# Kernel tuning notes

Hardware: AMD Instinct MI355X
Metric: run time of the kernel (lower is better)

The kernel has to match this reference:

```python
import jax, jax.numpy as jnp
import numpy as np

IN_DIM, HID, B, T = 64, 256, 256, 512


def setup_inputs() -> dict:
    key = jax.random.key(0)
    ks = jax.random.split(key, 12)
    s_in = 1.0 / np.sqrt(HID)
    d = {
        "x": jax.random.normal(ks[0], (B, T, IN_DIM), dtype=jnp.float32),
        # PyTorch LSTM layer 0 params (gate order i,f,g,o)
        "W_ih0": jax.random.uniform(ks[1], (4 * HID, IN_DIM), jnp.float32, -s_in, s_in),
        "W_hh0": jax.random.uniform(ks[2], (4 * HID, HID), jnp.float32, -s_in, s_in),
        "b_ih0": jax.random.uniform(ks[3], (4 * HID,), jnp.float32, -s_in, s_in),
        "b_hh0": jax.random.uniform(ks[4], (4 * HID,), jnp.float32, -s_in, s_in),
        # layer 1
        "W_ih1": jax.random.uniform(ks[5], (4 * HID, HID), jnp.float32, -s_in, s_in),
        "W_hh1": jax.random.uniform(ks[6], (4 * HID, HID), jnp.float32, -s_in, s_in),
        "b_ih1": jax.random.uniform(ks[7], (4 * HID,), jnp.float32, -s_in, s_in),
        "b_hh1": jax.random.uniform(ks[8], (4 * HID,), jnp.float32, -s_in, s_in),
        # linear head
        "W_head": jax.random.uniform(ks[9], (1, HID), jnp.float32, -s_in, s_in),
        "b_head": jax.random.uniform(ks[10], (1,), jnp.float32, -s_in, s_in),
    }
    return d


def _lstm_layer(x, W_ih, W_hh, b_ih, b_hh):
    """x: [B,T,Din] -> (outputs [B,T,H], last hidden [B,H]). PyTorch gate order i,f,g,o."""
    Bb = x.shape[0]
    H = W_hh.shape[1]
    # precompute input contribution for all timesteps: [B,T,4H]
    xg = jnp.einsum("btd,gd->btg", x, W_ih) + b_ih + b_hh

    def step(carry, xg_t):
        h, c = carry
        gates = xg_t + h @ W_hh.T  # [B,4H]
        i, f, g, o = jnp.split(gates, 4, axis=-1)
        c = jax.nn.sigmoid(f) * c + jax.nn.sigmoid(i) * jnp.tanh(g)
        h = jax.nn.sigmoid(o) * jnp.tanh(c)
        return (h, c), h

    init = (jnp.zeros((Bb, H), x.dtype), jnp.zeros((Bb, H), x.dtype))
    (h_last, _), hs = jax.lax.scan(step, init, jnp.swapaxes(xg, 0, 1))
    return jnp.swapaxes(hs, 0, 1), h_last


def reference(x, W_ih0, W_hh0, b_ih0, b_hh0, W_ih1, W_hh1, b_ih1, b_hh1, W_head, b_head):
    out0, _ = _lstm_layer(x, W_ih0, W_hh0, b_ih0, b_hh0)
    # eval mode: inter-layer dropout is identity
    _, h_last = _lstm_layer(out0, W_ih1, W_hh1, b_ih1, b_hh1)
    return h_last @ W_head.T + b_head  # [B, 1]
```

## Files before the change

kernel.cpp:

```cpp
#include <hip/hip_runtime.h>
#include <stdint.h>


#define TT 512

typedef short short8 __attribute__((ext_vector_type(8)));
typedef float f32x4 __attribute__((ext_vector_type(4)));
typedef uint32_t u32x4 __attribute__((ext_vector_type(4)));
typedef uint32_t u32x2 __attribute__((ext_vector_type(2)));

#define H0_OFF    0
#define H1_OFF    1048576
#define FLAGS_OFF 1572864
#define WS_BYTES  (1572864 + 4096)

static __device__ __forceinline__ unsigned short f2bf(float f) {
  uint32_t u = __float_as_uint(f);
  u += 0x7fffu + ((u >> 16) & 1u);
  return (unsigned short)(u >> 16);
}
static __device__ __forceinline__ float bf2f(unsigned short b) {
  return __uint_as_float(((uint32_t)b) << 16);
}

static __device__ __forceinline__ void pack_hilo(float4 a, float4 b,
                                                 short8& hi, short8& lo) {
  float v[8] = {a.x, a.y, a.z, a.w, b.x, b.y, b.z, b.w};
#pragma unroll
  for (int i = 0; i < 8; ++i) {
    unsigned short h = f2bf(v[i]);
    hi[i] = (short)h;
    lo[i] = (short)f2bf(v[i] - bf2f(h));
  }
}

static __device__ __forceinline__ float sigf(float x) {
  return 1.0f / (1.0f + __expf(-x));
}
static __device__ __forceinline__ float tanh_fast(float x) {
  float xx = fminf(fmaxf(x, -15.0f), 15.0f);
  float e = __expf(2.0f * xx);
  return (e - 1.0f) / (e + 1.0f);
}

static __device__ __forceinline__ f32x4 mfma16(short8 a, short8 b, f32x4 c) {
  return __builtin_amdgcn_mfma_f32_16x16x32_bf16(a, b, c, 0, 0, 0);
}

static __device__ __forceinline__ short8 u2s8(u32x4 v) {
  union { u32x4 u; short8 s; } c; c.u = v; return c.s;
}

static __device__ __forceinline__ u32x4 ldx4_cc(const uint32_t* p) {
  u32x4 r;
  asm volatile("global_load_dwordx4 %0, %1, off sc0 sc1"
               : "=&v"(r) : "v"(p) : "memory");
  return r;
}
static __device__ __forceinline__ void stx2_cc(uint32_t* p, u32x2 v) {
  asm volatile("global_store_dwordx2 %0, %1, off sc0 sc1"
               :: "v"(p), "v"(v) : "memory");
}
static __device__ __forceinline__ void vm_drain() {
  asm volatile("s_waitcnt vmcnt(0)" ::: "memory");
}

static __device__ __forceinline__ void wait_flags(const uint32_t* fl,
                                                  uint32_t tgt) {
  const uint32_t* p = fl + (threadIdx.x & 15);
  int guard = 0;
  for (;;) {
    uint32_t v = __hip_atomic_load(p, __ATOMIC_RELAXED,
                                   __HIP_MEMORY_SCOPE_AGENT);
    if (__all((int)(v >= tgt))) break;
    if (++guard > (1 << 20)) break;
  }
}

__global__ __launch_bounds__(256, 1) void lstm2_kernel(
    const float* __restrict__ x,
    const float* __restrict__ Wih0, const float* __restrict__ Whh0,
    const float* __restrict__ bih0, const float* __restrict__ bhh0,
    const float* __restrict__ Wih1, const float* __restrict__ Whh1,
    const float* __restrict__ bih1, const float* __restrict__ bhh1,
    const float* __restrict__ Whead, const float* __restrict__ bhead,
    float* __restrict__ out, uint8_t* __restrict__ ws)
{
  const int bid   = blockIdx.x;
  const int bg    = bid & 7;
  const int role  = bid >> 3;
  const int layer = role >> 4;
  const int fs    = role & 15;
  const int f0    = fs << 4;
  const int tid   = threadIdx.x;
  const int wave  = tid >> 6;
  const int lane  = tid & 63;
  const int mh    = (wave >> 1) & 1;
  const int kh    = wave & 1;
  const int lrow  = lane & 15;
  const int kg    = lane >> 4;

  uint32_t* h0d = (uint32_t*)(ws + H0_OFF);
  uint32_t* h1d = (uint32_t*)(ws + H1_OFF);
  uint32_t* flags  = (uint32_t*)(ws + FLAGS_OFF);
  uint32_t* flags0 = flags + bg * 32;
  uint32_t* flags1 = flags + bg * 32 + 16;

  __shared__ f32x4 pg[2][4][64];
  __shared__ uint32_t hbuf[32][17];

  short8 Bhi[2][4][4], Blo[2][4][4];
  short8 Xhi[4], Xlo[4];
  float bias[4] = {0, 0, 0, 0};
  float wh = 0.0f, bh = 0.0f;

  const float* WH = layer ? Whh1 : Whh0;
  const float* BI = layer ? bih1 : bih0;
  const float* BH = layer ? bhh1 : bhh0;

#pragma unroll
  for (int kt = 0; kt < 4; ++kt) {
#pragma unroll
    for (int n = 0; n < 4; ++n) {
      const int R = n * 256 + f0 + lrow;
      const int k = kh * 128 + kt * 32 + kg * 8;
      const float* p = WH + (size_t)R * 256 + k;
      pack_hilo(*(const float4*)p, *(const float4*)(p + 4),
                Bhi[1][kt][n], Blo[1][kt][n]);
    }
  }
  if (layer == 1) {
#pragma unroll
    for (int kt = 0; kt < 4; ++kt) {
#pragma unroll
      for (int n = 0; n < 4; ++n) {
        const int R = n * 256 + f0 + lrow;
        const int k = kh * 128 + kt * 32 + kg * 8;
        const float* p = Wih1 + (size_t)R * 256 + k;
        pack_hilo(*(const float4*)p, *(const float4*)(p + 4),
                  Bhi[0][kt][n], Blo[0][kt][n]);
      }
    }
  } else {
#pragma unroll
    for (int n = 0; n < 4; ++n) {
      const int R = n * 256 + f0 + lrow;
      const float* p = Wih0 + (size_t)R * 64 + kh * 32 + kg * 8;
      pack_hilo(*(const float4*)p, *(const float4*)(p + 4), Xhi[n], Xlo[n]);
    }
  }
  if (kh == 0) {
#pragma unroll
    for (int n = 0; n < 4; ++n) {
      const int R = n * 256 + f0 + lrow;
      bias[n] = BI[R] + BH[R];
    }
    if (layer == 1) { wh = Whead[f0 + lrow]; bh = bhead[0]; }
  }

  const int e0s  = tid * 2;
  const int pp   = e0s >> 8;
  const int uls  = (e0s & 255) >> 2;
  const int sj0  = e0s & 3;
  const int srow = uls & 31;
  const int skc  = uls >> 5;
  const int scc  = skc * 8 + sj0 * 2;
  const int sug  = (fs * 2 + skc) * 32 + srow;

  float cst[4] = {0, 0, 0, 0};

  if (layer == 0) {
    const float* xbase =
        x + (size_t)(bg * 32 + mh * 16 + lrow) * TT * 64 + kh * 32 + kg * 8;
    for (int t = 0; t < TT; ++t) {
      float4 xa = *(const float4*)(xbase + (size_t)t * 64);
      float4 xb = *(const float4*)(xbase + (size_t)t * 64 + 4);
      short8 xhi, xlo;
      pack_hilo(xa, xb, xhi, xlo);

      f32x4 acc[4];
#pragma unroll
      for (int n = 0; n < 4; ++n) {
        acc[n] = (f32x4)(0.0f);
        acc[n] = mfma16(xhi, Xhi[n], acc[n]);
        acc[n] = mfma16(xlo, Xhi[n], acc[n]);
        acc[n] = mfma16(xhi, Xlo[n], acc[n]);
      }

      if (t > 0) wait_flags(flags0, (uint32_t)t);
      {
        const uint32_t* base =
            h0d + (size_t)((((t - 1) & 3) * 8 + bg) * 2) * 4096;
        u32x4 vh[4], vl[4];
#pragma unroll
        for (int kt = 0; kt < 4; ++kt) {
          const int unit = (kh * 16 + kt * 4 + kg) * 32 + mh * 16 + lrow;
          vh[kt] = ldx4_cc(base + unit * 4);
          vl[kt] = ldx4_cc(base + 4096 + unit * 4);
        }
        vm_drain();
        __builtin_amdgcn_sched_barrier(0);
#pragma unroll
        for (int kt = 0; kt < 4; ++kt) {
          short8 ahi = u2s8(vh[kt]);
          short8 alo = u2s8(vl[kt]);
#pragma unroll
          for (int n = 0; n < 4; ++n) {
            acc[n] = mfma16(ahi, Bhi[1][kt][n], acc[n]);
            acc[n] = mfma16(alo, Bhi[1][kt][n], acc[n]);
            acc[n] = mfma16(ahi, Blo[1][kt][n], acc[n]);
          }
        }
      }

      if (kh == 1) {
#pragma unroll
        for (int n = 0; n < 4; ++n) pg[mh][n][lane] = acc[n];
      }
      __syncthreads();
      if (kh == 0) {
#pragma unroll
        for (int n = 0; n < 4; ++n) acc[n] += pg[mh][n][lane];
#pragma unroll
        for (int r = 0; r < 4; ++r) {
          float gi = acc[0][r] + bias[0];
          float gf = acc[1][r] + bias[1];
          float gg = acc[2][r] + bias[2];
          float go = acc[3][r] + bias[3];
          float cc = sigf(gf) * cst[r] + sigf(gi) * tanh_fast(gg);
          cst[r] = cc;
          float hv = sigf(go) * tanh_fast(cc);
          const int b = mh * 16 + kg * 4 + r;
          unsigned short hh = f2bf(hv);
          unsigned short hl = f2bf(hv - bf2f(hh));
          hbuf[b][lrow] = (uint32_t)hh | ((uint32_t)hl << 16);
        }
      }
      __syncthreads();
      if (t >= 4) wait_flags(flags1, (uint32_t)(t - 3));
      {
        uint32_t* base = h0d + (size_t)(((t & 3) * 8 + bg) * 2) * 4096;
        uint32_t* dstp = (pp == 0) ? base : base + 4096;
        uint32_t w0 = hbuf[srow][scc],     w1 = hbuf[srow][scc + 1];
        uint32_t w2 = hbuf[srow][scc + 2], w3 = hbuf[srow][scc + 3];
        u32x2 val;
        if (pp == 0) {
          val[0] = (w0 & 0xffffu) | (w1 << 16);
          val[1] = (w2 & 0xffffu) | (w3 << 16);
        } else {
          val[0] = (w0 >> 16) | (w1 & 0xffff0000u);
          val[1] = (w2 >> 16) | (w3 & 0xffff0000u);
        }
        stx2_cc(dstp + sug * 4 + sj0, val);
      }
      vm_drain();
      __syncthreads();
      if (tid == 0)
        __hip_atomic_store(flags0 + fs, (uint32_t)(t + 1), __ATOMIC_RELAXED,
                           __HIP_MEMORY_SCOPE_AGENT);
    }
  } else {
    for (int s = 0; s < TT; ++s) {
      if (s > 0) wait_flags(flags1, (uint32_t)s);
      const uint32_t* b1 =
          h1d + (size_t)((((s - 1) & 1) * 8 + bg) * 2) * 4096;
      u32x4 y1h[4], y1l[4];
#pragma unroll
      for (int kt = 0; kt < 4; ++kt) {
        const int unit = (kh * 16 + kt * 4 + kg) * 32 + mh * 16 + lrow;
        y1h[kt] = ldx4_cc(b1 + unit * 4);
        y1l[kt] = ldx4_cc(b1 + 4096 + unit * 4);
      }

      wait_flags(flags0, (uint32_t)(s + 1));
      const uint32_t* b0 = h0d + (size_t)(((s & 3) * 8 + bg) * 2) * 4096;
      u32x4 y0h[4], y0l[4];
#pragma unroll
      for (int kt = 0; kt < 4; ++kt) {
        const int unit = (kh * 16 + kt * 4 + kg) * 32 + mh * 16 + lrow;
        y0h[kt] = ldx4_cc(b0 + unit * 4);
        y0l[kt] = ldx4_cc(b0 + 4096 + unit * 4);
      }
      vm_drain();
      __builtin_amdgcn_sched_barrier(0);

      f32x4 acc[4];
#pragma unroll
      for (int n = 0; n < 4; ++n) acc[n] = (f32x4)(0.0f);

#pragma unroll
      for (int kt = 0; kt < 4; ++kt) {
        short8 ahi = u2s8(y0h[kt]);
        short8 alo = u2s8(y0l[kt]);
#pragma unroll
        for (int n = 0; n < 4; ++n) {
          acc[n] = mfma16(ahi, Bhi[0][kt][n], acc[n]);
          acc[n] = mfma16(alo, Bhi[0][kt][n], acc[n]);
          acc[n] = mfma16(ahi, Blo[0][kt][n], acc[n]);
        }
      }
#pragma unroll
      for (int kt = 0; kt < 4; ++kt) {
        short8 ahi = u2s8(y1h[kt]);
        short8 alo = u2s8(y1l[kt]);
#pragma unroll
        for (int n = 0; n < 4; ++n) {
          acc[n] = mfma16(ahi, Bhi[1][kt][n], acc[n]);
          acc[n] = mfma16(alo, Bhi[1][kt][n], acc[n]);
          acc[n] = mfma16(ahi, Blo[1][kt][n], acc[n]);
        }
      }

      if (kh == 1) {
#pragma unroll
        for (int n = 0; n < 4; ++n) pg[mh][n][lane] = acc[n];
      }
      __syncthreads();
      if (kh == 0) {
#pragma unroll
        for (int n = 0; n < 4; ++n) acc[n] += pg[mh][n][lane];
        float hva[4];
#pragma unroll
        for (int r = 0; r < 4; ++r) {
          float gi = acc[0][r] + bias[0];
          float gf = acc[1][r] + bias[1];
          float gg = acc[2][r] + bias[2];
          float go = acc[3][r] + bias[3];
          float cc = sigf(gf) * cst[r] + sigf(gi) * tanh_fast(gg);
          cst[r] = cc;
          float hv = sigf(go) * tanh_fast(cc);
          hva[r] = hv;
          const int b = mh * 16 + kg * 4 + r;
          unsigned short hh = f2bf(hv);
          unsigned short hl = f2bf(hv - bf2f(hh));
          hbuf[b][lrow] = (uint32_t)hh | ((uint32_t)hl << 16);
        }
        if (s == TT - 1) {
#pragma unroll
          for (int r = 0; r < 4; ++r) {
            float v = hva[r] * wh;
            v += __shfl_xor(v, 1);
            v += __shfl_xor(v, 2);
            v += __shfl_xor(v, 4);
            v += __shfl_xor(v, 8);
            if (lrow == 0) {
              float add = v + (fs == 0 ? bh : 0.0f);
              atomicAdd(out + bg * 32 + mh * 16 + kg * 4 + r, add);
            }
          }
        }
      }
      __syncthreads();
      {
        uint32_t* base = h1d + (size_t)(((s & 1) * 8 + bg) * 2) * 4096;
        uint32_t* dstp = (pp == 0) ? base : base + 4096;
        uint32_t w0 = hbuf[srow][scc],     w1 = hbuf[srow][scc + 1];
        uint32_t w2 = hbuf[srow][scc + 2], w3 = hbuf[srow][scc + 3];
        u32x2 val;
        if (pp == 0) {
          val[0] = (w0 & 0xffffu) | (w1 << 16);
          val[1] = (w2 & 0xffffu) | (w3 << 16);
        } else {
          val[0] = (w0 >> 16) | (w1 & 0xffff0000u);
          val[1] = (w2 >> 16) | (w3 & 0xffff0000u);
        }
        stx2_cc(dstp + sug * 4 + sj0, val);
      }
      vm_drain();
      __syncthreads();
      if (tid == 0)
        __hip_atomic_store(flags1 + fs, (uint32_t)(s + 1), __ATOMIC_RELAXED,
                           __HIP_MEMORY_SCOPE_AGENT);
    }
  }
}

extern "C" void kernel_launch(void* const* d_in, const int* in_sizes, int n_in,
                              void* d_out, int out_size, void* d_ws, size_t ws_size,
                              hipStream_t stream) {
  (void)in_sizes; (void)n_in; (void)ws_size;
  const float* x     = (const float*)d_in[0];
  const float* Wih0  = (const float*)d_in[1];
  const float* Whh0  = (const float*)d_in[2];
  const float* bih0  = (const float*)d_in[3];
  const float* bhh0  = (const float*)d_in[4];
  const float* Wih1  = (const float*)d_in[5];
  const float* Whh1  = (const float*)d_in[6];
  const float* bih1  = (const float*)d_in[7];
  const float* bhh1  = (const float*)d_in[8];
  const float* Whead = (const float*)d_in[9];
  const float* bhead = (const float*)d_in[10];

  hipMemsetAsync(d_ws, 0, WS_BYTES, stream);
  hipMemsetAsync(d_out, 0, (size_t)out_size * sizeof(float), stream);
  lstm2_kernel<<<dim3(256), dim3(256), 0, stream>>>(
      x, Wih0, Whh0, bih0, bhh0, Wih1, Whh1, bih1, bhh1, Whead, bhead,
      (float*)d_out, (uint8_t*)d_ws);
}
```

Measured before the change: 3.003 ms.

## Use per-wave flag slots with combined polling and split-wait MFMA overlap

Each wave now publishes its own progress flag, which removes the trailing block barrier before the flag store. A single wave polls both layer-0 and layer-1 flags at once with 64-bit loads and s_sleep backoff, then a block barrier releases the other waves. Loads are reordered so MFMAs on the first half of the hidden-state data start while the rest is still in flight (partial vmcnt waits). This reduces synchronisation latency in the recurrent loop, at the cost of more polling traffic and a larger flag area.

Measured after the change: 2.884 ms. 4.0% less time.

```diff
diff --git a/kernel.cpp b/kernel.cpp
--- a/kernel.cpp
+++ b/kernel.cpp
@@ -12,7 +12,7 @@
 #define H0_OFF    0
 #define H1_OFF    1048576
 #define FLAGS_OFF 1572864
-#define WS_BYTES  (1572864 + 4096)
+#define WS_BYTES  (1572864 + 8 * 4096)
 
 static __device__ __forceinline__ unsigned short f2bf(float f) {
   uint32_t u = __float_as_uint(f);
@@ -64,16 +64,27 @@
 static __device__ __forceinline__ void vm_drain() {
   asm volatile("s_waitcnt vmcnt(0)" ::: "memory");
 }
-
-static __device__ __forceinline__ void wait_flags(const uint32_t* fl,
-                                                  uint32_t tgt) {
-  const uint32_t* p = fl + (threadIdx.x & 15);
+static __device__ __forceinline__ void vm_wait4() {
+  asm volatile("s_waitcnt vmcnt(4)" ::: "memory");
+}
+static __device__ __forceinline__ void vm_wait8() {
+  asm volatile("s_waitcnt vmcnt(8)" ::: "memory");
+}
+
+static __device__ __forceinline__ void poll_combined(const uint32_t* fbg,
+                                                     uint32_t tgt0,
+                                                     uint32_t tgt1,
+                                                     int lane) {
+  const uint64_t* p = (const uint64_t*)fbg + lane;
+  const uint32_t tgt = (lane < 32) ? tgt0 : tgt1;
   int guard = 0;
   for (;;) {
-    uint32_t v = __hip_atomic_load(p, __ATOMIC_RELAXED,
+    uint64_t v = __hip_atomic_load(p, __ATOMIC_RELAXED,
                                    __HIP_MEMORY_SCOPE_AGENT);
-    if (__all((int)(v >= tgt))) break;
+    uint32_t a = (uint32_t)v, b = (uint32_t)(v >> 32);
+    if (__all((int)(a >= tgt && b >= tgt))) break;
     if (++guard > (1 << 20)) break;
+    __builtin_amdgcn_s_sleep(2);
   }
 }
 
@@ -102,9 +113,8 @@
 
   uint32_t* h0d = (uint32_t*)(ws + H0_OFF);
   uint32_t* h1d = (uint32_t*)(ws + H1_OFF);
-  uint32_t* flags  = (uint32_t*)(ws + FLAGS_OFF);
-  uint32_t* flags0 = flags + bg * 32;
-  uint32_t* flags1 = flags + bg * 32 + 16;
+  uint32_t* fbg = (uint32_t*)(ws + FLAGS_OFF) + bg * 1024;
+  uint32_t* my_slot = fbg + (layer ? 64 : 0) + fs * 4 + wave;
 
   __shared__ f32x4 pg[2][4][64];
   __shared__ uint32_t hbuf[32][17];
@@ -187,29 +197,43 @@
         acc[n] = mfma16(xhi, Xlo[n], acc[n]);
       }
 
-      if (t > 0) wait_flags(flags0, (uint32_t)t);
+      if (t > 0) {
+        if (wave == 0)
+          poll_combined(fbg, (uint32_t)t,
+                        (t >= 4) ? (uint32_t)(t - 3) : 0u, lane);
+      }
+      __syncthreads();
+
       {
         const uint32_t* base =
             h0d + (size_t)((((t - 1) & 3) * 8 + bg) * 2) * 4096;
+        const int unitc = (kh * 16 + kg) * 32 + mh * 16 + lrow;
         u32x4 vh[4], vl[4];
 #pragma unroll
+        for (int kt = 0; kt < 4; ++kt)
+          vh[kt] = ldx4_cc(base + (unitc + kt * 4 * 32) * 4);
+#pragma unroll
+        for (int kt = 0; kt < 4; ++kt)
+          vl[kt] = ldx4_cc(base + 4096 + (unitc + kt * 4 * 32) * 4);
+        vm_wait4();
+        __builtin_amdgcn_sched_barrier(0);
+#pragma unroll
         for (int kt = 0; kt < 4; ++kt) {
-          const int unit = (kh * 16 + kt * 4 + kg) * 32 + mh * 16 + lrow;
-          vh[kt] = ldx4_cc(base + unit * 4);
-          vl[kt] = ldx4_cc(base + 4096 + unit * 4);
+          short8 ahi = u2s8(vh[kt]);
+#pragma unroll
+          for (int n = 0; n < 4; ++n) {
+            acc[n] = mfma16(ahi, Bhi[1][kt][n], acc[n]);
+            acc[n] = mfma16(ahi, Blo[1][kt][n], acc[n]);
+          }
         }
         vm_drain();
         __builtin_amdgcn_sched_barrier(0);
 #pragma unroll
         for (int kt = 0; kt < 4; ++kt) {
-          short8 ahi = u2s8(vh[kt]);
           short8 alo = u2s8(vl[kt]);
 #pragma unroll
-          for (int n = 0; n < 4; ++n) {
-            acc[n] = mfma16(ahi, Bhi[1][kt][n], acc[n]);
+          for (int n = 0; n < 4; ++n)
             acc[n] = mfma16(alo, Bhi[1][kt][n], acc[n]);
-            acc[n] = mfma16(ahi, Blo[1][kt][n], acc[n]);
-          }
         }
       }
 
@@ -237,7 +261,6 @@
         }
       }
       __syncthreads();
-      if (t >= 4) wait_flags(flags1, (uint32_t)(t - 3));
       {
         uint32_t* base = h0d + (size_t)(((t & 3) * 8 + bg) * 2) * 4096;
         uint32_t* dstp = (pp == 0) ? base : base + 4096;
@@ -254,40 +277,53 @@
         stx2_cc(dstp + sug * 4 + sj0, val);
       }
       vm_drain();
-      __syncthreads();
-      if (tid == 0)
-        __hip_atomic_store(flags0 + fs, (uint32_t)(t + 1), __ATOMIC_RELAXED,
+      if (lane == 0)
+        __hip_atomic_store(my_slot, (uint32_t)(t + 1), __ATOMIC_RELAXED,
                            __HIP_MEMORY_SCOPE_AGENT);
     }
   } else {
     for (int s = 0; s < TT; ++s) {
-      if (s > 0) wait_flags(flags1, (uint32_t)s);
+      if (wave == 0)
+        poll_combined(fbg, (uint32_t)(s + 1), (uint32_t)s, lane);
+      __syncthreads();
+
       const uint32_t* b1 =
           h1d + (size_t)((((s - 1) & 1) * 8 + bg) * 2) * 4096;
-      u32x4 y1h[4], y1l[4];
+      const uint32_t* b0 = h0d + (size_t)(((s & 3) * 8 + bg) * 2) * 4096;
+      const int unitc = (kh * 16 + kg) * 32 + mh * 16 + lrow;
+      u32x4 y1h[4], y1l[4], y0h[4], y0l[4];
+#pragma unroll
+      for (int kt = 0; kt < 4; ++kt)
+        y1h[kt] = ldx4_cc(b1 + (unitc + kt * 4 * 32) * 4);
+#pragma unroll
+      for (int kt = 0; kt < 4; ++kt)
+        y1l[kt] = ldx4_cc(b1 + 4096 + (unitc + kt * 4 * 32) * 4);
+#pragma unroll
+      for (int kt = 0; kt < 4; ++kt)
+        y0h[kt] = ldx4_cc(b0 + (unitc + kt * 4 * 32) * 4);
+#pragma unroll
+      for (int kt = 0; kt < 4; ++kt)
+        y0l[kt] = ldx4_cc(b0 + 4096 + (unitc + kt * 4 * 32) * 4);
+
+      f32x4 acc[4];
+#pragma unroll
+      for (int n = 0; n < 4; ++n) acc[n] = (f32x4)(0.0f);
+
+      vm_wait8();
+      __builtin_amdgcn_sched_barrier(0);
 #pragma unroll
       for (int kt = 0; kt < 4; ++kt) {
-        const int unit = (kh * 16 + kt * 4 + kg) * 32 + mh * 16 + lrow;
-        y1h[kt] = ldx4_cc(b1 + unit * 4);
-        y1l[kt] = ldx4_cc(b1 + 4096 + unit * 4);
-      }
-
-      wait_flags(flags0, (uint32_t)(s + 1));
-      const uint32_t* b0 = h0d + (size_t)(((s & 3) * 8 + bg) * 2) * 4096;
-      u32x4 y0h[4], y0l[4];
-#pragma unroll
-      for (int kt = 0; kt < 4; ++kt) {
-        const int unit = (kh * 16 + kt * 4 + kg) * 32 + mh * 16 + lrow;
-        y0h[kt] = ldx4_cc(b0 + unit * 4);
-        y0l[kt] = ldx4_cc(b0 + 4096 + unit * 4);
+        short8 ahi = u2s8(y1h[kt]);
+        short8 alo = u2s8(y1l[kt]);
+#pragma unroll
+        for (int n = 0; n < 4; ++n) {
+          acc[n] = mfma16(ahi, Bhi[1][kt][n], acc[n]);
+          acc[n] = mfma16(alo, Bhi[1][kt][n], acc[n]);
+          acc[n] = mfma16(ahi, Blo[1][kt][n], acc[n]);
+        }
       }
       vm_drain();
       __builtin_amdgcn_sched_barrier(0);
-
-      f32x4 acc[4];
-#pragma unroll
-      for (int n = 0; n < 4; ++n) acc[n] = (f32x4)(0.0f);
-
 #pragma unroll
       for (int kt = 0; kt < 4; ++kt) {
         short8 ahi = u2s8(y0h[kt]);
@@ -297,17 +333,6 @@
           acc[n] = mfma16(ahi, Bhi[0][kt][n], acc[n]);
           acc[n] = mfma16(alo, Bhi[0][kt][n], acc[n]);
           acc[n] = mfma16(ahi, Blo[0][kt][n], acc[n]);
-        }
-      }
-#pragma unroll
-      for (int kt = 0; kt < 4; ++kt) {
-        short8 ahi = u2s8(y1h[kt]);
-        short8 alo = u2s8(y1l[kt]);
-#pragma unroll
-        for (int n = 0; n < 4; ++n) {
-          acc[n] = mfma16(ahi, Bhi[1][kt][n], acc[n]);
-          acc[n] = mfma16(alo, Bhi[1][kt][n], acc[n]);
-          acc[n] = mfma16(ahi, Blo[1][kt][n], acc[n]);
         }
       }
 
@@ -367,9 +392,8 @@
         stx2_cc(dstp + sug * 4 + sj0, val);
       }
       vm_drain();
-      __syncthreads();
-      if (tid == 0)
-        __hip_atomic_store(flags1 + fs, (uint32_t)(s + 1), __ATOMIC_RELAXED,
+      if (lane == 0)
+        __hip_atomic_store(my_slot, (uint32_t)(s + 1), __ATOMIC_RELAXED,
                            __HIP_MEMORY_SCOPE_AGENT);
     }
   }
```
